# Kernel optimization log

Hardware: AMD Instinct MI355X
Metric: run time of the kernel (lower is better)

Reference implementation:

```python
import jax, jax.numpy as jnp
import numpy as np

B, C, H, W = 32, 1024, 48, 24
P = 3            # num_parts
IC = C // 8      # inter_channels for position attention
PH = H // P      # part height


def setup_inputs() -> dict:
    key = jax.random.key(0)
    ks = jax.random.split(key, 16)
    s = 0.02
    return {
        "x": jax.random.normal(ks[0], (B, C, H, W), jnp.float32),
        "modality": jax.random.randint(ks[1], (B,), 0, 2),
        # per-part 1x1 conv weights (stacked over parts)
        "Wq": jax.random.normal(ks[2], (P, IC, C), jnp.float32) * s,
        "bq": jnp.zeros((P, IC), jnp.float32),
        "Wk": jax.random.normal(ks[3], (P, IC, C), jnp.float32) * s,
        "bk": jnp.zeros((P, IC), jnp.float32),
        "Wv": jax.random.normal(ks[4], (P, C, C), jnp.float32) * s,
        "bv": jnp.zeros((P, C), jnp.float32),
        # gamma residual scales (torch inits to 0; random so output differs from x)
        "gamma_pa": jax.random.normal(ks[5], (P,), jnp.float32) * 0.1,
        "gamma_ca": jax.random.normal(ks[6], (P,), jnp.float32) * 0.1,
        # modality gate: Linear(1,64) -> ReLU -> Linear(64,P) -> Sigmoid
        "gW1": jax.random.normal(ks[7], (64, 1), jnp.float32) * 0.01,
        "gb1": jnp.zeros((64,), jnp.float32),
        "gW2": jax.random.normal(ks[8], (P, 64), jnp.float32) * 0.01,
        "gb2": jnp.zeros((P,), jnp.float32),
    }


def _part_dual_attn(part, Wq, bq, Wk, bk, Wv, bv, g_pa, g_ca):
    # part: [B, C, ph, W]
    b, c, ph, w = part.shape
    n = ph * w
    xf = part.reshape(b, c, n)  # [B,C,N]
    # --- Position attention (PAM) ---
    q = jnp.einsum('oc,bcn->bno', Wq, xf) + bq            # [B,N,IC]
    k = jnp.einsum('oc,bcn->bon', Wk, xf) + bk[:, None]   # [B,IC,N]
    attn = jax.nn.softmax(jnp.einsum('bno,bom->bnm', q, k), axis=-1)  # [B,N,N]
    v = jnp.einsum('oc,bcn->bon', Wv, xf) + bv[:, None]   # [B,C,N]
    pa = jnp.einsum('bcn,bmn->bcm', v, attn).reshape(part.shape)
    pa = g_pa * pa + part
    # --- Channel attention (CAM) with max-shifted softmax ---
    e = jnp.einsum('bcn,bdn->bcd', xf, xf)                # [B,C,C]
    e = jnp.max(e, axis=-1, keepdims=True) - e
    ca_attn = jax.nn.softmax(e, axis=-1)
    ca = jnp.einsum('bcd,bdn->bcn', ca_attn, xf).reshape(part.shape)
    ca = g_ca * ca + part
    return pa + ca


def reference(x, modality, Wq, bq, Wk, bk, Wv, bv, gamma_pa, gamma_ca, gW1, gb1, gW2, gb2):
    b = x.shape[0]
    # modality gate -> per-sample per-part blend weights [B,P]
    m = modality.astype(jnp.float32)[:, None]
    h = jax.nn.relu(m @ gW1.T + gb1)
    w_gate = jax.nn.sigmoid(h @ gW2.T + gb2)              # [B,P]
    # split into P horizontal parts: [P,B,C,ph,W]
    parts = x.reshape(b, C, P, PH, W).transpose(2, 0, 1, 3, 4)
    part_outs = jax.vmap(_part_dual_attn)(parts, Wq, bq, Wk, bk, Wv, bv, gamma_pa, gamma_ca)
    wp = w_gate.T[:, :, None, None, None]                 # [P,B,1,1,1]
    blended = parts * (1.0 - wp) + part_outs * wp         # [P,B,C,ph,W]
    return blended.transpose(1, 2, 0, 3, 4).reshape(b, C, H, W)
```

## Files before the change

kernel.cpp:

```cpp
#include <hip/hip_runtime.h>
#include <hip/hip_bf16.h>
#include <cstdint>

constexpr int kB  = 32;
constexpr int kC  = 1024;
constexpr int kH  = 48;
constexpr int kW  = 24;
constexpr int kP  = 3;
constexpr int kPH = 16;
constexpr int kN  = kPH * kW;
constexpr int kHW = kH * kW;
constexpr int64_t kCHW = (int64_t)kC * kHW;

typedef __attribute__((ext_vector_type(8))) short short8b;
typedef __attribute__((ext_vector_type(4))) float f32x4;

__device__ __forceinline__ void gl_lds16(const void* g, void* l) {
    __builtin_amdgcn_global_load_lds(
        (const __attribute__((address_space(1))) void*)g,
        (__attribute__((address_space(3))) void*)l, 16, 0, 0);
}

__device__ __forceinline__ void swz_block(int& bx, int& by, int& bz) {
    const int gx = gridDim.x, gy = gridDim.y, gz = gridDim.z;
    if ((gz & 7) == 0) {
        const int tpp = gx * gy;
        const int L   = (blockIdx.z * gy + blockIdx.y) * gx + blockIdx.x;
        const int xcd = L & 7;
        const int idx = L >> 3;
        const int ppx = gz >> 3;
        const int pairL = idx / tpp;
        const int tile  = idx - pairL * tpp;
        bz = xcd * ppx + pairL;
        by = tile / gx;
        bx = tile - by * gx;
    } else {
        bx = blockIdx.x; by = blockIdx.y; bz = blockIdx.z;
    }
}

#define WAIT10()      asm volatile("s_waitcnt vmcnt(10)" ::: "memory")
#define WAIT8()       asm volatile("s_waitcnt vmcnt(8)" ::: "memory")
#define WAIT5()       asm volatile("s_waitcnt vmcnt(5)" ::: "memory")
#define WAIT0()       asm volatile("s_waitcnt vmcnt(0)" ::: "memory")
#define RAW_BARRIER() asm volatile("s_barrier" ::: "memory")
#define SFENCE()      __builtin_amdgcn_sched_barrier(0)

__global__ void gate_kernel(const int* __restrict__ modality,
                            const float* __restrict__ gW1, const float* __restrict__ gb1,
                            const float* __restrict__ gW2, const float* __restrict__ gb2,
                            const float* __restrict__ gpa, const float* __restrict__ gca,
                            const float* __restrict__ bq, const float* __restrict__ bk,
                            float* __restrict__ wg, float* __restrict__ cpa,
                            float* __restrict__ cca, float* __restrict__ bqk)
{
    const int t = threadIdx.x;
    if (t < 768) {
        const int p = t >> 8, o = t & 255;
        bqk[t] = (o < 128) ? bq[p * 128 + o] : bk[p * 128 + (o - 128)];
    }
    if (t < kB * kP) {
        const int b = t / kP, p = t % kP;
        const float m = (float)modality[b];
        float acc = gb2[p];
        #pragma unroll
        for (int j = 0; j < 64; ++j) {
            float h = fmaxf(fmaf(m, gW1[j], gb1[j]), 0.0f);
            acc = fmaf(gW2[p * 64 + j], h, acc);
        }
        const float w = 1.0f / (1.0f + __expf(-acc));
        wg[t]  = w;
        cpa[t] = w * gpa[p];
        cca[t] = w * gca[p];
    }
}

__global__ __launch_bounds__(256)
void wcast_kernel(const float* __restrict__ Wq, const float* __restrict__ Wk,
                  const float* __restrict__ Wv,
                  __hip_bfloat16* __restrict__ Wqkb, __hip_bfloat16* __restrict__ Wvb)
{
    const int64_t i = (int64_t)blockIdx.x * 256 + threadIdx.x;
    if (i < 196608) {
        const int64_t e = i * 4;
        const int p = (int)(e / 262144);
        const int rem = (int)(e % 262144);
        const int o = rem / 1024, c = rem % 1024;
        const float* s = (o < 128) ? (Wq + (int64_t)p * 131072 + (int64_t)o * 1024 + c)
                                   : (Wk + (int64_t)p * 131072 + (int64_t)(o - 128) * 1024 + c);
        float4 v = *(const float4*)s;
        __hip_bfloat16* d = Wqkb + e;
        d[0] = __float2bfloat16(v.x); d[1] = __float2bfloat16(v.y);
        d[2] = __float2bfloat16(v.z); d[3] = __float2bfloat16(v.w);
    } else if (i < 196608 + 786432) {
        const int64_t e = (i - 196608) * 4;
        float4 v = *(const float4*)(Wv + e);
        __hip_bfloat16* d = Wvb + e;
        d[0] = __float2bfloat16(v.x); d[1] = __float2bfloat16(v.y);
        d[2] = __float2bfloat16(v.z); d[3] = __float2bfloat16(v.w);
    }
}

__global__ void zeroz_kernel(float* __restrict__ Z)
{
    Z[(int64_t)blockIdx.x * 1024 + threadIdx.x] = 0.0f;
}

__global__ __launch_bounds__(256)
void cast_tr_kernel(const float* __restrict__ x,
                    __hip_bfloat16* __restrict__ xfb,
                    __hip_bfloat16* __restrict__ xfT)
{
    int bx, by, bz;
    swz_block(bx, by, bz);
    const int j = bz;
    const int bb = j / kP, pp = j % kP;
    const float* src = x + (int64_t)bb * kCHW + pp * kN;
    const int c0 = bx * 32, n0 = by * 32;
    __shared__ float tile[32][33];
    const int tx = threadIdx.x & 31, ty = threadIdx.x >> 5;
    #pragma unroll
    for (int r = 0; r < 4; ++r) {
        const int cl = ty * 4 + r;
        const int c = c0 + cl;
        float v = src[(int64_t)c * kHW + n0 + tx];
        xfb[(int64_t)j * 393216 + (int64_t)c * kN + n0 + tx] = __float2bfloat16(v);
        tile[tx][cl] = v;
    }
    __syncthreads();
    #pragma unroll
    for (int r = 0; r < 4; ++r) {
        const int nl = ty * 4 + r;
        xfT[(int64_t)j * 393216 + (int64_t)(n0 + nl) * kC + c0 + tx] =
            __float2bfloat16(tile[nl][tx]);
    }
}

template<int BIAS>
__global__ __launch_bounds__(256, 2)
void mm_kernel(const __hip_bfloat16* __restrict__ A0, int64_t aSB, int64_t aSP, int lda,
               const __hip_bfloat16* __restrict__ B0, int64_t bSB, int64_t bSP, int ldb,
               __hip_bfloat16* __restrict__ C0, int64_t cSB, int64_t cSP, int ldc,
               const float* __restrict__ bias0, int biasSP, int K)
{
    __shared__ char lds[65536];

    int bx, by, bz;
    swz_block(bx, by, bz);
    const int j = bz, bb = j / kP, pp = j % kP;
    const char* Ab = (const char*)(A0 + (int64_t)bb * aSB + (int64_t)pp * aSP);
    const char* Bb = (const char*)(B0 + (int64_t)bb * bSB + (int64_t)pp * bSP);
    const int m0 = bx * 128, n0 = by * 128;
    const int t = threadIdx.x, lane = t & 63, wv = t >> 6;
    const int wm = (wv & 1) * 64, wn = (wv >> 1) * 64;
    const size_t ldab = (size_t)lda * 2, ldbb = (size_t)ldb * 2;

    const int rr   = wv * 8 + (lane >> 3);
    const int gsrc = ((lane & 7) ^ (lane >> 3)) * 16;
    const int lrow = (wv * 8 + (lane >> 3)) * 128 + (lane & 7) * 16;

    auto STAGE = [&](int buf, int k0) {
        const char* Asrc = Ab + (size_t)(m0 + rr) * ldab + (size_t)k0 * 2 + gsrc;
        const char* Bsrc = Bb + (size_t)(n0 + rr) * ldbb + (size_t)k0 * 2 + gsrc;
        char* As = lds + buf * 32768;
        char* Bs = As + 16384;
        #pragma unroll
        for (int i = 0; i < 4; ++i) {
            gl_lds16(Asrc + (size_t)i * 32 * ldab, As + i * 4096 + lrow);
            gl_lds16(Bsrc + (size_t)i * 32 * ldbb, Bs + i * 4096 + lrow);
        }
    };

    f32x4 acc[4][4];
    #pragma unroll
    for (int a = 0; a < 4; ++a)
        #pragma unroll
        for (int b = 0; b < 4; ++b) acc[a][b] = (f32x4){0.f, 0.f, 0.f, 0.f};

    const int nk = K >> 6;
    STAGE(0, 0);
    int cur = 0;
    for (int k = 0; k < nk; ++k) {
        if (k + 1 < nk) { STAGE(cur ^ 1, (k + 1) << 6); WAIT8(); }
        else            { WAIT0(); }
        SFENCE();
        RAW_BARRIER();
        const char* As = lds + cur * 32768;
        const char* Bs = As + 16384;
        #pragma unroll
        for (int kk = 0; kk < 2; ++kk) {
            const int gpos = ((kk * 4 + (lane >> 4)) ^ (lane & 7)) * 16;
            short8b af[4], bf[4];
            #pragma unroll
            for (int f = 0; f < 4; ++f) {
                af[f] = *(const short8b*)(As + (wm + f * 16 + (lane & 15)) * 128 + gpos);
                bf[f] = *(const short8b*)(Bs + (wn + f * 16 + (lane & 15)) * 128 + gpos);
            }
            #pragma unroll
            for (int fm = 0; fm < 4; ++fm)
                #pragma unroll
                for (int fn = 0; fn < 4; ++fn)
                    acc[fm][fn] = __builtin_amdgcn_mfma_f32_16x16x32_bf16(
                        af[fm], bf[fn], acc[fm][fn], 0, 0, 0);
        }
        RAW_BARRIER();
        cur ^= 1;
    }

    __hip_bfloat16* Cm = C0 + (int64_t)bb * cSB + (int64_t)pp * cSP;
    #pragma unroll
    for (int fn = 0; fn < 4; ++fn) {
        const int col = n0 + wn + fn * 16 + (lane & 15);
        const float cb = (BIAS == 2) ? bias0[pp * biasSP + col] : 0.0f;
        #pragma unroll
        for (int fm = 0; fm < 4; ++fm)
            #pragma unroll
            for (int jr = 0; jr < 4; ++jr) {
                const int row = m0 + wm + fm * 16 + (lane >> 4) * 4 + jr;
                Cm[(int64_t)row * ldc + col] = __float2bfloat16(acc[fm][fn][jr] + cb);
            }
    }
}

__global__ __launch_bounds__(256, 2)
void ecam_kernel(const __hip_bfloat16* __restrict__ xfb,
                 __hip_bfloat16* __restrict__ eb,
                 float* __restrict__ Z)
{
    __shared__ char lds[65536];

    int bx, by, bz;
    swz_block(bx, by, bz);
    const int j = bz;
    int bi = 0;
    while ((bi + 1) * (bi + 2) / 2 <= bx) ++bi;
    const int bj = bx - bi * (bi + 1) / 2;
    const char* Ab = (const char*)(xfb + (int64_t)j * 393216);
    const int m0 = bi * 128, n0 = bj * 128;
    const int t = threadIdx.x, lane = t & 63, wv = t >> 6;
    const int wm = (wv & 1) * 64, wn = (wv >> 1) * 64;
    constexpr size_t ldab = 768;

    const int rr   = wv * 8 + (lane >> 3);
    const int gsrc = ((lane & 7) ^ (lane >> 3)) * 16;
    const int lrow = (wv * 8 + (lane >> 3)) * 128 + (lane & 7) * 16;

    auto STAGE = [&](int buf, int k0) {
        const char* Asrc = Ab + (size_t)(m0 + rr) * ldab + (size_t)k0 * 2 + gsrc;
        const char* Bsrc = Ab + (size_t)(n0 + rr) * ldab + (size_t)k0 * 2 + gsrc;
        char* As = lds + buf * 32768;
        char* Bs = As + 16384;
        #pragma unroll
        for (int i = 0; i < 4; ++i) {
            gl_lds16(Asrc + (size_t)i * 32 * ldab, As + i * 4096 + lrow);
            gl_lds16(Bsrc + (size_t)i * 32 * ldab, Bs + i * 4096 + lrow);
        }
    };

    f32x4 acc[4][4];
    #pragma unroll
    for (int a = 0; a < 4; ++a)
        #pragma unroll
        for (int b = 0; b < 4; ++b) acc[a][b] = (f32x4){0.f, 0.f, 0.f, 0.f};

    STAGE(0, 0);
    int cur = 0;
    for (int k = 0; k < 6; ++k) {
        if (k + 1 < 6) { STAGE(cur ^ 1, (k + 1) << 6); WAIT8(); }
        else           { WAIT0(); }
        SFENCE();
        RAW_BARRIER();
        const char* As = lds + cur * 32768;
        const char* Bs = As + 16384;
        #pragma unroll
        for (int kk = 0; kk < 2; ++kk) {
            const int gpos = ((kk * 4 + (lane >> 4)) ^ (lane & 7)) * 16;
            short8b af[4], bf[4];
            #pragma unroll
            for (int f = 0; f < 4; ++f) {
                af[f] = *(const short8b*)(As + (wm + f * 16 + (lane & 15)) * 128 + gpos);
                bf[f] = *(const short8b*)(Bs + (wn + f * 16 + (lane & 15)) * 128 + gpos);
            }
            #pragma unroll
            for (int fm = 0; fm < 4; ++fm)
                #pragma unroll
                for (int fn = 0; fn < 4; ++fn)
                    acc[fm][fn] = __builtin_amdgcn_mfma_f32_16x16x32_bf16(
                        af[fm], bf[fn], acc[fm][fn], 0, 0, 0);
        }
        RAW_BARRIER();
        cur ^= 1;
    }

    #pragma unroll
    for (int fm = 0; fm < 4; ++fm)
        #pragma unroll
        for (int fn = 0; fn < 4; ++fn)
            #pragma unroll
            for (int jr = 0; jr < 4; ++jr)
                acc[fm][fn][jr] = __expf(-60.f - acc[fm][fn][jr]);

    __hip_bfloat16* Cm = eb + (int64_t)j * 1048576;
    float* Zp = Z + (int64_t)j * 1024;

    #pragma unroll
    for (int fm = 0; fm < 4; ++fm)
        #pragma unroll
        for (int jr = 0; jr < 4; ++jr) {
            const int row = m0 + wm + fm * 16 + (lane >> 4) * 4 + jr;
            float v = 0.f;
            #pragma unroll
            for (int fn = 0; fn < 4; ++fn) {
                const int col = n0 + wn + fn * 16 + (lane & 15);
                Cm[(int64_t)row * 1024 + col] = __float2bfloat16(acc[fm][fn][jr]);
                v += acc[fm][fn][jr];
            }
            v += __shfl_xor(v, 1);
            v += __shfl_xor(v, 2);
            v += __shfl_xor(v, 4);
            v += __shfl_xor(v, 8);
            if ((lane & 15) == 0) atomicAdd(Zp + row, v);
        }

    if (bi != bj) {
        #pragma unroll
        for (int fn = 0; fn < 4; ++fn) {
            const int col = n0 + wn + fn * 16 + (lane & 15);
            float v2 = 0.f;
            #pragma unroll
            for (int fm = 0; fm < 4; ++fm) {
                const int row0 = m0 + wm + fm * 16 + (lane >> 4) * 4;
                __hip_bfloat16 h0 = __float2bfloat16(acc[fm][fn][0]);
                __hip_bfloat16 h1 = __float2bfloat16(acc[fm][fn][1]);
                __hip_bfloat16 h2 = __float2bfloat16(acc[fm][fn][2]);
                __hip_bfloat16 h3 = __float2bfloat16(acc[fm][fn][3]);
                ushort4 w4;
                w4.x = *(ushort*)&h0; w4.y = *(ushort*)&h1;
                w4.z = *(ushort*)&h2; w4.w = *(ushort*)&h3;
                *(ushort4*)((ushort*)Cm + (int64_t)col * 1024 + row0) = w4;
                v2 += (acc[fm][fn][0] + acc[fm][fn][1]) +
                      (acc[fm][fn][2] + acc[fm][fn][3]);
            }
            v2 += __shfl_xor(v2, 16);
            v2 += __shfl_xor(v2, 32);
            if ((lane >> 4) == 0) atomicAdd(Zp + col, v2);
        }
    }
}

__global__ __launch_bounds__(512, 1)
void ep_cam_kernel(const __hip_bfloat16* __restrict__ Wvb,
                   const __hip_bfloat16* __restrict__ yTb,
                   const __hip_bfloat16* __restrict__ eb,
                   const __hip_bfloat16* __restrict__ xfT,
                   const float* __restrict__ Z,
                   const float* __restrict__ x,
                   float* __restrict__ out,
                   const float* __restrict__ wg,
                   const float* __restrict__ cpa,
                   const float* __restrict__ cca,
                   const float* __restrict__ bv)
{
    extern __shared__ char lds[];

    int bx, by, bz;
    swz_block(bx, by, bz);
    const int j = bz, bb = j / kP, pp = j % kP;
    const int m0 = bx * 512, n0 = by * 128;
    const int t = threadIdx.x, lane = t & 63, wv = t >> 6;
    const int wm = (wv & 3) * 128, wn = (wv >> 2) * 64;

    const int rr   = t >> 2;
    const int gsrc = ((t & 3) ^ ((t >> 3) & 3)) * 16;
    const int ldst = wv * 1024 + lane * 16;

    const char* AbW = (const char*)(Wvb + (int64_t)pp * 1048576);
    const char* AbE = (const char*)(eb  + (int64_t)j  * 1048576);
    const char* BbY = (const char*)(yTb + (int64_t)j * 393216);
    const char* BbX = (const char*)(xfT + (int64_t)j * 393216);

    auto STAGE = [&](int buf, int g) {
        const char* A = (g < 32) ? AbE : AbW;
        const char* B = (g < 32) ? BbX : BbY;
        const size_t k0b = (size_t)(g & 31) * 64;
        const char* Asrc = A + (size_t)(m0 + rr) * 2048 + k0b + gsrc;
        const char* Bsrc = B + (size_t)(n0 + rr) * 2048 + k0b + gsrc;
        char* As = lds + (size_t)buf * 40960;
        char* Bs = As + 32768;
        #pragma unroll
        for (int i = 0; i < 4; ++i)
            gl_lds16(Asrc + (size_t)i * 128 * 2048, As + i * 8192 + ldst);
        gl_lds16(Bsrc, Bs + ldst);
    };

    const float cfc = cca[j];
    const float* Zp = Z + (int64_t)j * 1024;
    f32x4 zsc[8];
    #pragma unroll
    for (int fm = 0; fm < 8; ++fm)
        #pragma unroll
        for (int jr = 0; jr < 4; ++jr) {
            const int row = m0 + wm + fm * 16 + (lane >> 4) * 4 + jr;
            zsc[fm][jr] = cfc / Zp[row];
        }

    f32x4 acc[8][4];
    #pragma unroll
    for (int a = 0; a < 8; ++a)
        #pragma unroll
        for (int b = 0; b < 4; ++b) acc[a][b] = (f32x4){0.f, 0.f, 0.f, 0.f};

    const int gpos = ((lane >> 4) ^ ((lane >> 1) & 3)) * 16;

    STAGE(0, 0);
    STAGE(1, 1);
    int cur = 0;
    #pragma unroll 1
    for (int g = 0; g < 64; ++g) {
        if (g < 62) {
            int nb = cur + 2; if (nb >= 3) nb -= 3;
            STAGE(nb, g + 2);
            WAIT10();
        } else if (g == 62) { WAIT5(); }
        else                { WAIT0(); }
        SFENCE();
        RAW_BARRIER();
        if (g == 32) {
            #pragma unroll
            for (int fm = 0; fm < 8; ++fm)
                #pragma unroll
                for (int jr = 0; jr < 4; ++jr) {
                    const float zs = zsc[fm][jr];
                    #pragma unroll
                    for (int fn = 0; fn < 4; ++fn) acc[fm][fn][jr] *= zs;
                }
        }
        const char* As = lds + (size_t)cur * 40960;
        const char* Bs = As + 32768;
        short8b bf[4];
        #pragma unroll
        for (int f = 0; f < 4; ++f)
            bf[f] = *(const short8b*)(Bs + (wn + f * 16 + (lane & 15)) * 64 + gpos);
        {
            short8b af[4];
            #pragma unroll
            for (int f = 0; f < 4; ++f)
                af[f] = *(const short8b*)(As + (wm + f * 16 + (lane & 15)) * 64 + gpos);
            #pragma unroll
            for (int fm = 0; fm < 4; ++fm)
                #pragma unroll
                for (int fn = 0; fn < 4; ++fn)
                    acc[fm][fn] = __builtin_amdgcn_mfma_f32_16x16x32_bf16(
                        af[fm], bf[fn], acc[fm][fn], 0, 0, 0);
        }
        {
            short8b af[4];
            #pragma unroll
            for (int f = 0; f < 4; ++f)
                af[f] = *(const short8b*)(As + (wm + (f + 4) * 16 + (lane & 15)) * 64 + gpos);
            #pragma unroll
            for (int fm = 0; fm < 4; ++fm)
                #pragma unroll
                for (int fn = 0; fn < 4; ++fn)
                    acc[fm + 4][fn] = __builtin_amdgcn_mfma_f32_16x16x32_bf16(
                        af[fm], bf[fn], acc[fm + 4][fn], 0, 0, 0);
        }
        RAW_BARRIER();
        if (++cur == 3) cur = 0;
    }

    const float gsc = 1.0f + wg[j];
    const float cfp = cpa[j];
    const float* Xm = x   + (int64_t)bb * kCHW + pp * kN;
    float*       Om = out + (int64_t)bb * kCHW + pp * kN;
    #pragma unroll
    for (int fm = 0; fm < 8; ++fm)
        #pragma unroll
        for (int jr = 0; jr < 4; ++jr) {
            const int row = m0 + wm + fm * 16 + (lane >> 4) * 4 + jr;
            const float rb = cfp * bv[pp * 1024 + row];
            #pragma unroll
            for (int fn = 0; fn < 4; ++fn) {
                const int col = n0 + wn + fn * 16 + (lane & 15);
                const int64_t off = (int64_t)row * kHW + col;
                Om[off] = fmaf(gsc, Xm[off], acc[fm][fn][jr] + rb);
            }
        }
}

__global__ __launch_bounds__(64) void sm_pam(__hip_bfloat16* __restrict__ buf,
                                             const float* __restrict__ scale,
                                             int chPairs)
{
    const int L = blockIdx.x;
    int pair, row;
    if ((chPairs & 7) == 0) {
        const int xcd = L & 7, idx = L >> 3;
        pair = xcd * (chPairs >> 3) + idx / kN;
        row  = idx % kN;
    } else { pair = L / kN; row = L % kN; }
    __hip_bfloat16* rp = buf + (int64_t)pair * (kN * kN) + (int64_t)row * kN;
    const int t = threadIdx.x;
    float v[6];
    float mx = -3.402823466e38f;
    #pragma unroll
    for (int r = 0; r < 6; ++r) {
        v[r] = __bfloat162float(rp[t + 64 * r]);
        mx = fmaxf(mx, v[r]);
    }
    #pragma unroll
    for (int off = 32; off > 0; off >>= 1) mx = fmaxf(mx, __shfl_xor(mx, off));
    float s = 0.0f;
    #pragma unroll
    for (int r = 0; r < 6; ++r) { v[r] = __expf(v[r] - mx); s += v[r]; }
    #pragma unroll
    for (int off = 32; off > 0; off >>= 1) s += __shfl_xor(s, off);
    const float inv = scale[pair] / s;
    #pragma unroll
    for (int r = 0; r < 6; ++r) rp[t + 64 * r] = __float2bfloat16(v[r] * inv);
}

extern "C" void kernel_launch(void* const* d_in, const int* in_sizes, int n_in,
                              void* d_out, int out_size, void* d_ws, size_t ws_size,
                              hipStream_t stream)
{
    const float* x   = (const float*)d_in[0];
    const int*   mod = (const int*)d_in[1];
    const float* Wq  = (const float*)d_in[2];
    const float* bq  = (const float*)d_in[3];
    const float* Wk  = (const float*)d_in[4];
    const float* bk  = (const float*)d_in[5];
    const float* Wv  = (const float*)d_in[6];
    const float* bv  = (const float*)d_in[7];
    const float* gpa = (const float*)d_in[8];
    const float* gca = (const float*)d_in[9];
    const float* gW1 = (const float*)d_in[10];
    const float* gb1 = (const float*)d_in[11];
    const float* gW2 = (const float*)d_in[12];
    const float* gb2 = (const float*)d_in[13];
    float* out = (float*)d_out;

    const int chList[6] = {96, 48, 24, 12, 6, 3};
    int CH = 3;
    for (int i = 0; i < 6; ++i) {
        size_t need = 7868544ull + (size_t)chList[i] * 4952064ull;
        if (need <= ws_size) { CH = chList[i]; break; }
    }
    const int NCHUNK = 96 / CH;

    char* ws = (char*)d_ws;
    __hip_bfloat16* Wqkb = (__hip_bfloat16*)(ws + 0);
    __hip_bfloat16* Wvb  = (__hip_bfloat16*)(ws + 1572864);
    float* bqk = (float*)(ws + 7864320);
    float* wg  = (float*)(ws + 7867392);
    float* cpa = (float*)(ws + 7867776);
    float* cca = (float*)(ws + 7868160);
    __hip_bfloat16* xfT   = (__hip_bfloat16*)(ws + 7868544);
    __hip_bfloat16* xfb   = xfT   + (int64_t)CH * 393216;
    __hip_bfloat16* qkT   = xfb   + (int64_t)CH * 393216;
    __hip_bfloat16* attnb = qkT   + (int64_t)CH * 98304;
    __hip_bfloat16* yTb   = attnb + (int64_t)CH * 147456;
    __hip_bfloat16* eb    = yTb   + (int64_t)CH * 393216;
    float*          Zbuf  = (float*)(eb + (int64_t)CH * 1048576);

    gate_kernel<<<1, 768, 0, stream>>>(mod, gW1, gb1, gW2, gb2, gpa, gca, bq, bk,
                                       wg, cpa, cca, bqk);
    wcast_kernel<<<3840, 256, 0, stream>>>(Wq, Wk, Wv, Wqkb, Wvb);

    for (int ch = 0; ch < NCHUNK; ++ch) {
        const int pair0 = ch * CH;
        const int b0 = pair0 / kP;
        const float* xc   = x   + (int64_t)b0 * kCHW;
        float*       outc = out + (int64_t)b0 * kCHW;

        cast_tr_kernel<<<dim3(32, 12, CH), 256, 0, stream>>>(xc, xfb, xfT);
        zeroz_kernel<<<CH, 1024, 0, stream>>>(Zbuf);

        mm_kernel<2><<<dim3(3, 2, CH), 256, 0, stream>>>(
            xfT, 3 * 393216, 393216, 1024,
            Wqkb, 0, 262144, 1024,
            qkT, 3 * 98304, 98304, 256,
            bqk, 256, 1024);
        mm_kernel<0><<<dim3(3, 3, CH), 256, 0, stream>>>(
            qkT, 3 * 98304, 98304, 256,
            qkT + 128, 3 * 98304, 98304, 256,
            attnb, 3 * 147456, 147456, 384,
            nullptr, 0, 128);
        sm_pam<<<CH * kN, 64, 0, stream>>>(attnb, cpa + pair0, CH);
        mm_kernel<0><<<dim3(3, 8, CH), 256, 0, stream>>>(
            attnb, 3 * 147456, 147456, 384,
            xfb, 3 * 393216, 393216, 384,
            yTb, 3 * 393216, 393216, 1024,
            nullptr, 0, 384);
        ecam_kernel<<<dim3(36, 1, CH), 256, 0, stream>>>(xfb, eb, Zbuf);
        ep_cam_kernel<<<dim3(2, 3, CH), 512, 122880, stream>>>(
            Wvb, yTb, eb, xfT, Zbuf, xc, outc,
            wg + pair0, cpa + pair0, cca + pair0, bv);
    }
}
```

Measured before the change: 605.3 us.

## Retile CAM epilogue GEMM, vectorize cast-transpose, pack softmax rows per block

The cast/transpose kernel now loads float4 per thread over 128-wide column tiles and writes packed bf16 pairs for the transposed copy, cutting the number of memory instructions. ep_cam_kernel goes from 512-thread, 512-row tiles at one block per CU to 256-thread, 256-row tiles at two blocks per CU. The smaller LDS stages mean the vmcnt wait counts are adjusted to match. The PAM softmax packs four rows into each 256-thread block, which drops the XCD-aware row mapping. In exchange, B tiles are reloaded more often across the extra M blocks.

```diff
diff --git a/kernel.cpp b/kernel.cpp
--- a/kernel.cpp
+++ b/kernel.cpp
@@ -39,9 +39,9 @@
     }
 }
 
-#define WAIT10()      asm volatile("s_waitcnt vmcnt(10)" ::: "memory")
+#define WAIT12()      asm volatile("s_waitcnt vmcnt(12)" ::: "memory")
 #define WAIT8()       asm volatile("s_waitcnt vmcnt(8)" ::: "memory")
-#define WAIT5()       asm volatile("s_waitcnt vmcnt(5)" ::: "memory")
+#define WAIT6()       asm volatile("s_waitcnt vmcnt(6)" ::: "memory")
 #define WAIT0()       asm volatile("s_waitcnt vmcnt(0)" ::: "memory")
 #define RAW_BARRIER() asm volatile("s_barrier" ::: "memory")
 #define SFENCE()      __builtin_amdgcn_sched_barrier(0)
@@ -116,23 +116,33 @@
     const int j = bz;
     const int bb = j / kP, pp = j % kP;
     const float* src = x + (int64_t)bb * kCHW + pp * kN;
-    const int c0 = bx * 32, n0 = by * 32;
-    __shared__ float tile[32][33];
+    const int c0 = bx * 32, n0 = by * 128;
+    __shared__ float tile[32][129];
     const int tx = threadIdx.x & 31, ty = threadIdx.x >> 5;
     #pragma unroll
     for (int r = 0; r < 4; ++r) {
         const int cl = ty * 4 + r;
-        const int c = c0 + cl;
-        float v = src[(int64_t)c * kHW + n0 + tx];
-        xfb[(int64_t)j * 393216 + (int64_t)c * kN + n0 + tx] = __float2bfloat16(v);
-        tile[tx][cl] = v;
+        const int c  = c0 + cl;
+        float4 v = *(const float4*)(src + (int64_t)c * kHW + n0 + tx * 4);
+        __hip_bfloat16 h0 = __float2bfloat16(v.x), h1 = __float2bfloat16(v.y);
+        __hip_bfloat16 h2 = __float2bfloat16(v.z), h3 = __float2bfloat16(v.w);
+        ushort4 hv;
+        hv.x = *(ushort*)&h0; hv.y = *(ushort*)&h1;
+        hv.z = *(ushort*)&h2; hv.w = *(ushort*)&h3;
+        *(ushort4*)((ushort*)xfb + (int64_t)j * 393216 + (int64_t)c * kN + n0 + tx * 4) = hv;
+        tile[cl][tx * 4 + 0] = v.x; tile[cl][tx * 4 + 1] = v.y;
+        tile[cl][tx * 4 + 2] = v.z; tile[cl][tx * 4 + 3] = v.w;
     }
     __syncthreads();
-    #pragma unroll
-    for (int r = 0; r < 4; ++r) {
-        const int nl = ty * 4 + r;
-        xfT[(int64_t)j * 393216 + (int64_t)(n0 + nl) * kC + c0 + tx] =
-            __float2bfloat16(tile[nl][tx]);
+    const int cc = (threadIdx.x & 15) * 2;
+    const int nr = threadIdx.x >> 4;
+    #pragma unroll
+    for (int r = 0; r < 8; ++r) {
+        const int nl = r * 16 + nr;
+        __hip_bfloat16 h0 = __float2bfloat16(tile[cc][nl]);
+        __hip_bfloat16 h1 = __float2bfloat16(tile[cc + 1][nl]);
+        ushort2 h2; h2.x = *(ushort*)&h0; h2.y = *(ushort*)&h1;
+        *(ushort2*)((ushort*)xfT + (int64_t)j * 393216 + (int64_t)(n0 + nl) * kC + c0 + cc) = h2;
     }
 }
 
@@ -348,7 +358,7 @@
     }
 }
 
-__global__ __launch_bounds__(512, 1)
+__global__ __launch_bounds__(256, 2)
 void ep_cam_kernel(const __hip_bfloat16* __restrict__ Wvb,
                    const __hip_bfloat16* __restrict__ yTb,
                    const __hip_bfloat16* __restrict__ eb,
@@ -366,13 +376,12 @@
     int bx, by, bz;
     swz_block(bx, by, bz);
     const int j = bz, bb = j / kP, pp = j % kP;
-    const int m0 = bx * 512, n0 = by * 128;
+    const int m0 = bx * 256, n0 = by * 128;
     const int t = threadIdx.x, lane = t & 63, wv = t >> 6;
-    const int wm = (wv & 3) * 128, wn = (wv >> 2) * 64;
+    const int wm = (wv & 1) * 128, wn = (wv >> 1) * 64;
 
     const int rr   = t >> 2;
     const int gsrc = ((t & 3) ^ ((t >> 3) & 3)) * 16;
-    const int ldst = wv * 1024 + lane * 16;
 
     const char* AbW = (const char*)(Wvb + (int64_t)pp * 1048576);
     const char* AbE = (const char*)(eb  + (int64_t)j  * 1048576);
@@ -385,12 +394,14 @@
         const size_t k0b = (size_t)(g & 31) * 64;
         const char* Asrc = A + (size_t)(m0 + rr) * 2048 + k0b + gsrc;
         const char* Bsrc = B + (size_t)(n0 + rr) * 2048 + k0b + gsrc;
-        char* As = lds + (size_t)buf * 40960;
-        char* Bs = As + 32768;
+        char* As = lds + (size_t)buf * 24576;
+        char* Bs = As + 16384;
         #pragma unroll
         for (int i = 0; i < 4; ++i)
-            gl_lds16(Asrc + (size_t)i * 128 * 2048, As + i * 8192 + ldst);
-        gl_lds16(Bsrc, Bs + ldst);
+            gl_lds16(Asrc + (size_t)i * 64 * 2048, As + i * 4096 + t * 16);
+        #pragma unroll
+        for (int i = 0; i < 2; ++i)
+            gl_lds16(Bsrc + (size_t)i * 64 * 2048, Bs + i * 4096 + t * 16);
     };
 
     const float cfc = cca[j];
@@ -420,8 +431,8 @@
         if (g < 62) {
             int nb = cur + 2; if (nb >= 3) nb -= 3;
             STAGE(nb, g + 2);
-            WAIT10();
-        } else if (g == 62) { WAIT5(); }
+            WAIT12();
+        } else if (g == 62) { WAIT6(); }
         else                { WAIT0(); }
         SFENCE();
         RAW_BARRIER();
@@ -435,8 +446,8 @@
                     for (int fn = 0; fn < 4; ++fn) acc[fm][fn][jr] *= zs;
                 }
         }
-        const char* As = lds + (size_t)cur * 40960;
-        const char* Bs = As + 32768;
+        const char* As = lds + (size_t)cur * 24576;
+        const char* Bs = As + 16384;
         short8b bf[4];
         #pragma unroll
         for (int f = 0; f < 4; ++f)
@@ -488,19 +499,14 @@
         }
 }
 
-__global__ __launch_bounds__(64) void sm_pam(__hip_bfloat16* __restrict__ buf,
-                                             const float* __restrict__ scale,
-                                             int chPairs)
-{
-    const int L = blockIdx.x;
-    int pair, row;
-    if ((chPairs & 7) == 0) {
-        const int xcd = L & 7, idx = L >> 3;
-        pair = xcd * (chPairs >> 3) + idx / kN;
-        row  = idx % kN;
-    } else { pair = L / kN; row = L % kN; }
+__global__ __launch_bounds__(256) void sm_pam(__hip_bfloat16* __restrict__ buf,
+                                              const float* __restrict__ scale,
+                                              int chPairs)
+{
+    const int R = blockIdx.x * 4 + (threadIdx.x >> 6);
+    const int pair = R / kN, row = R % kN;
     __hip_bfloat16* rp = buf + (int64_t)pair * (kN * kN) + (int64_t)row * kN;
-    const int t = threadIdx.x;
+    const int t = threadIdx.x & 63;
     float v[6];
     float mx = -3.402823466e38f;
     #pragma unroll
@@ -573,7 +579,7 @@
         const float* xc   = x   + (int64_t)b0 * kCHW;
         float*       outc = out + (int64_t)b0 * kCHW;
 
-        cast_tr_kernel<<<dim3(32, 12, CH), 256, 0, stream>>>(xc, xfb, xfT);
+        cast_tr_kernel<<<dim3(32, 3, CH), 256, 0, stream>>>(xc, xfb, xfT);
         zeroz_kernel<<<CH, 1024, 0, stream>>>(Zbuf);
 
         mm_kernel<2><<<dim3(3, 2, CH), 256, 0, stream>>>(
@@ -586,14 +592,14 @@
             qkT + 128, 3 * 98304, 98304, 256,
             attnb, 3 * 147456, 147456, 384,
             nullptr, 0, 128);
-        sm_pam<<<CH * kN, 64, 0, stream>>>(attnb, cpa + pair0, CH);
+        sm_pam<<<CH * (kN / 4), 256, 0, stream>>>(attnb, cpa + pair0, CH);
         mm_kernel<0><<<dim3(3, 8, CH), 256, 0, stream>>>(
             attnb, 3 * 147456, 147456, 384,
             xfb, 3 * 393216, 393216, 384,
             yTb, 3 * 393216, 393216, 1024,
             nullptr, 0, 384);
         ecam_kernel<<<dim3(36, 1, CH), 256, 0, stream>>>(xfb, eb, Zbuf);
-        ep_cam_kernel<<<dim3(2, 3, CH), 512, 122880, stream>>>(
+        ep_cam_kernel<<<dim3(4, 3, CH), 256, 73728, stream>>>(
             Wvb, yTb, eb, xfT, Zbuf, xc, outc,
             wg + pair0, cpa + pair0, cca + pair0, bv);
     }
```

Result: faster. 549.6 us (-9.2%).
